# Kernel tuning notes

Hardware: AMD Instinct MI355X
Metric: run time of the kernel (lower is better)

## Reference

```python
import jax, jax.numpy as jnp
import numpy as np

B, N, M = 4, 1024, 4096
DQ, DC = 1024, 1024
H, DH = 16, 64
INNER = H * DH
SCALE = DH ** -0.5


def setup_inputs() -> dict:
    key = jax.random.key(0)
    ks = jax.random.split(key, 6)
    x = jax.random.normal(ks[0], (B, N, DQ), dtype=jnp.float32)
    context = jax.random.normal(ks[1], (B, M, DC), dtype=jnp.float32)
    mask = jax.random.bernoulli(ks[2], 0.9, (B, M))  # bool, True = keep
    # weights, scaled like default torch Linear init (~1/sqrt(fan_in))
    Wq = jax.random.normal(ks[3], (DQ, INNER), dtype=jnp.float32) / np.sqrt(DQ)
    Wkv = jax.random.normal(ks[4], (DC, 2 * INNER), dtype=jnp.float32) / np.sqrt(DC)
    Wo = jax.random.normal(ks[5], (INNER, DQ), dtype=jnp.float32) / np.sqrt(INNER)
    bo = jnp.zeros((DQ,), dtype=jnp.float32)
    return {"x": x, "context": context, "mask": mask,
            "Wq": Wq, "Wkv": Wkv, "Wo": Wo, "bo": bo}


def reference(x, context, mask, Wq, Wkv, Wo, bo):
    # projections
    q = x @ Wq                     # [b, n, h*d]
    kv = context @ Wkv             # [b, m, 2*h*d]
    k, v = jnp.split(kv, 2, axis=-1)
    # split heads: [b, s, h*d] -> [b, h, s, d]
    def heads(t):
        b, s, _ = t.shape
        return t.reshape(b, s, H, DH).transpose(0, 2, 1, 3)
    q, k, v = heads(q), heads(k), heads(v)
    sim = jnp.einsum('bhid,bhjd->bhij', q, k) * SCALE   # [b, h, n, m]
    max_neg = -jnp.finfo(sim.dtype).max
    sim = jnp.where(mask[:, None, None, :], sim, max_neg)
    sim = jnp.clip(sim, -5.0, 5.0)  # masked entries become exactly -5
    attn = jax.nn.softmax(sim, axis=-1)
    out = jnp.einsum('bhij,bhjd->bhid', attn, v)        # [b, h, n, d]
    out = out.transpose(0, 2, 1, 3).reshape(x.shape[0], x.shape[1], INNER)
    return out @ Wo + bo
```

## Files before the change

kernel.cpp:

```cpp
#include <hip/hip_runtime.h>
#include <hip/hip_bf16.h>


typedef __attribute__((ext_vector_type(8))) short short8;
typedef __attribute__((ext_vector_type(8))) unsigned short u16x8;
typedef __attribute__((ext_vector_type(4))) float f32x4;
typedef __attribute__((ext_vector_type(16))) float f32x16;

static __device__ __forceinline__ void gload_lds16(const void* g, void* l) {
  __builtin_amdgcn_global_load_lds((const __attribute__((address_space(1))) void*)g,
                                   (__attribute__((address_space(3))) void*)l, 16, 0, 0);
}

static __device__ __forceinline__ unsigned short f2bf(float f) {
  __hip_bfloat16 h = __float2bfloat16(f);
  unsigned short u;
  __builtin_memcpy(&u, &h, 2);
  return u;
}

static __device__ __forceinline__ float bf2f(unsigned short u) {
  unsigned int x = (unsigned int)u << 16;
  float f;
  __builtin_memcpy(&f, &x, 4);
  return f;
}

static __device__ __forceinline__ unsigned int pack_rnd(float a, float b) {
  unsigned int ua, ub;
  __builtin_memcpy(&ua, &a, 4);
  __builtin_memcpy(&ub, &b, 4);
  return __builtin_amdgcn_perm(ua + 0x8000u, ub + 0x8000u, 0x03020706u);
}

__global__ __launch_bounds__(256) void cast_bf16_kernel(const float* __restrict__ in,
                                                        unsigned short* __restrict__ out,
                                                        int n8) {
  int idx = blockIdx.x * 256 + threadIdx.x;
  int stride = gridDim.x * 256;
  for (int i = idx; i < n8; i += stride) {
    const float4* p = (const float4*)in + (size_t)i * 2;
    float4 a = p[0], b = p[1];
    u16x8 r;
    r[0] = f2bf(a.x); r[1] = f2bf(a.y); r[2] = f2bf(a.z); r[3] = f2bf(a.w);
    r[4] = f2bf(b.x); r[5] = f2bf(b.y); r[6] = f2bf(b.z); r[7] = f2bf(b.w);
    *((u16x8*)out + i) = r;
  }
}

__global__ __launch_bounds__(256) void mask_bias_kernel(const int* __restrict__ mask,
                                                        float* __restrict__ bias, int n) {
  int i = blockIdx.x * 256 + threadIdx.x;
  if (i < n) bias[i] = mask[i] ? 0.0f : -1e30f;
}

__global__ __launch_bounds__(256) void transpose_cast_kernel(const float* __restrict__ W,
                                                             unsigned short* __restrict__ Wt,
                                                             int K, int N) {
  __shared__ float tile[32][33];
  int n0 = blockIdx.x * 32, k0 = blockIdx.y * 32;
  int tx = threadIdx.x & 31, ty = threadIdx.x >> 5;
#pragma unroll
  for (int r = 0; r < 32; r += 8)
    tile[ty + r][tx] = W[(size_t)(k0 + ty + r) * N + n0 + tx];
  __syncthreads();
#pragma unroll
  for (int r = 0; r < 32; r += 8)
    Wt[(size_t)(n0 + ty + r) * K + k0 + tx] = f2bf(tile[tx][ty + r]);
}

template <int EPI>
__global__ __launch_bounds__(256, 2) void gemm_bt_kernel(
    const unsigned short* __restrict__ A, const unsigned short* __restrict__ Bt,
    int M, int N, int K,
    unsigned short* __restrict__ out0, unsigned short* __restrict__ out1,
    float* __restrict__ outF, const float* __restrict__ bias) {
  __shared__ unsigned short As[128 * 64];
  __shared__ unsigned short Bs[128 * 64];
  const int tid = threadIdx.x;
  const int l = tid & 63;
  const int lq = l & 15, g = l >> 4;
  const int w = tid >> 6;
  const int wr = w >> 1, wc = w & 1;
  const int nwg = gridDim.x * gridDim.y;
  const int idl = blockIdx.y * gridDim.x + blockIdx.x;
  const int lin = (idl & 7) * (nwg >> 3) + (idl >> 3);
  const int m0 = (lin / gridDim.x) * 128, n0 = (lin % gridDim.x) * 128;

  f32x4 acc[4][4] = {};

  for (int k0 = 0; k0 < K; k0 += 64) {
    __syncthreads();
#pragma unroll
    for (int t = 0; t < 4; ++t) {
      int c = t * 256 + tid;
      int row = c >> 3, cb = c & 7;
      int srcoff = (cb * 16) ^ ((row & 7) << 4);
      char* la = (char*)As + t * 4096 + (tid & 192) * 16;
      gload_lds16((const char*)(A + (size_t)(m0 + row) * K + k0) + srcoff, la);
      char* lb = (char*)Bs + t * 4096 + (tid & 192) * 16;
      gload_lds16((const char*)(Bt + (size_t)(n0 + row) * K + k0) + srcoff, lb);
    }
    __syncthreads();
#pragma unroll
    for (int ks = 0; ks < 2; ++ks) {
      short8 af[4], bfr[4];
#pragma unroll
      for (int mt = 0; mt < 4; ++mt) {
        int row = wr * 64 + mt * 16 + lq;
        af[mt] = *(const short8*)&As[row * 64 + ((ks * 32 + g * 8) ^ ((row & 7) << 3))];
      }
#pragma unroll
      for (int nt = 0; nt < 4; ++nt) {
        int row = wc * 64 + nt * 16 + lq;
        bfr[nt] = *(const short8*)&Bs[row * 64 + ((ks * 32 + g * 8) ^ ((row & 7) << 3))];
      }
#pragma unroll
      for (int mt = 0; mt < 4; ++mt)
#pragma unroll
        for (int nt = 0; nt < 4; ++nt)
          acc[mt][nt] =
              __builtin_amdgcn_mfma_f32_16x16x32_bf16(af[mt], bfr[nt], acc[mt][nt], 0, 0, 0);
    }
  }

#pragma unroll
  for (int mt = 0; mt < 4; ++mt) {
#pragma unroll
    for (int nt = 0; nt < 4; ++nt) {
      if (EPI == 1 && n0 >= 1024) {
        int colb = n0 - 1024 + wc * 64 + nt * 16 + lq;
        int h = colb >> 6, d = colb & 63;
        int rowb = m0 + wr * 64 + mt * 16 + g * 4;
        int b = rowb >> 12, mm = rowb & 4095;
        ushort4 pk;
        pk.x = f2bf(acc[mt][nt][0]);
        pk.y = f2bf(acc[mt][nt][1]);
        pk.z = f2bf(acc[mt][nt][2]);
        pk.w = f2bf(acc[mt][nt][3]);
        size_t off = (((size_t)(b * 16 + h) * 512 + (mm >> 3)) * 64 + d) * 8 + (mm & 7);
        *(ushort4*)&out1[off] = pk;
      } else {
#pragma unroll
        for (int r = 0; r < 4; ++r) {
          int row = m0 + wr * 64 + mt * 16 + g * 4 + r;
          int col = n0 + wc * 64 + nt * 16 + lq;
          float v = acc[mt][nt][r];
          if (EPI == 0) {
            int b = row >> 10, nq = row & 1023;
            int h = col >> 6, d = col & 63;
            out0[(((size_t)(b * 16 + h)) * 1024 + nq) * 64 + d] =
                f2bf(v * 0.18033688011112042f);
          } else if (EPI == 1) {
            int b = row >> 12, mm = row & 4095;
            int h = col >> 6, d = col & 63;
            size_t off = (((size_t)(b * 16 + h) * 8 + (d >> 3)) * 4096 + mm) * 8 + (d & 7);
            out0[off] = f2bf(v);
          } else {
            outF[(size_t)row * 1024 + col] = v + bias[col];
          }
        }
      }
    }
  }
}

__global__ __launch_bounds__(256, 3) void attn_kernel(
    const unsigned short* __restrict__ K2, const unsigned short* __restrict__ V2,
    const unsigned short* __restrict__ Q, const float* __restrict__ maskb,
    unsigned short* __restrict__ numP, float* __restrict__ denP) {
  __shared__ unsigned short Ks[8 * 128 * 8];
  __shared__ unsigned short Vt[16 * 64 * 8];

  const int tid = threadIdx.x;
  const int l = tid & 63, w = tid >> 6;
  const int lq = l & 31;
  const int hi = l >> 5;

  const int id = blockIdx.x;
  const int xcd = id & 7;
  const int kk = id >> 3;
  const int qi = kk & 7;
  const int pr = xcd * 32 + (kk >> 3);
  const int bh = pr & 63, js = pr >> 6;
  const int b = bh >> 4;
  const int q0 = qi * 128 + w * 32;

  const unsigned short* Qh = Q + (size_t)bh * 1024 * 64;
  const unsigned short* Kh = K2 + (size_t)bh * 8 * 4096 * 8;
  const unsigned short* Vh = V2 + (size_t)bh * 512 * 64 * 8;
  const float* bb = maskb + b * 4096;

  const float CLIP2 = 7.213475204444817f;

  short8 qf[4];
#pragma unroll
  for (int kc = 0; kc < 4; ++kc)
    qf[kc] = *(const short8*)&Qh[(size_t)(q0 + lq) * 64 + kc * 16 + hi * 8];

  f32x16 oacc[2] = {};
  float den = 0.f;

  for (int jt = js * 8; jt < js * 8 + 8; ++jt) {
    const int j0 = jt * 128;
    __syncthreads();
#pragma unroll
    for (int t = 0; t < 4; ++t) {
      int c = t * 256 + tid;
      int db = c >> 7, jj = c & 127;
      int sig = (jj & ~12) | ((jj & 4) << 1) | ((jj & 8) >> 1);
      char* lk = (char*)Ks + t * 4096 + (tid & 192) * 16;
      gload_lds16((const char*)(Kh + ((size_t)db * 4096 + j0 + sig) * 8), lk);
    }
#pragma unroll
    for (int t = 0; t < 4; ++t) {
      int c = t * 256 + tid;
      int jb = c >> 6, d = c & 63;
      char* lv = (char*)Vt + t * 4096 + (tid & 192) * 16;
      gload_lds16((const char*)(Vh + ((size_t)((j0 >> 3) + jb) * 64 + d) * 8), lv);
    }
    __syncthreads();

#pragma unroll
    for (int half = 0; half < 4; ++half) {
      f32x16 sacc;
#pragma unroll
      for (int bq = 0; bq < 4; ++bq) {
        f32x4 m4 = *(const f32x4*)&bb[j0 + half * 32 + ((bq & 1) << 2) + (hi << 3) +
                                      ((bq >> 1) << 4)];
        sacc[bq * 4 + 0] = m4[0];
        sacc[bq * 4 + 1] = m4[1];
        sacc[bq * 4 + 2] = m4[2];
        sacc[bq * 4 + 3] = m4[3];
      }
      __builtin_amdgcn_s_setprio(1);
#pragma unroll
      for (int kc = 0; kc < 4; ++kc) {
        short8 kf = *(const short8*)((const char*)Ks + (2 * kc + hi) * 2048 +
                                     (half * 32 + lq) * 16);
        sacc = __builtin_amdgcn_mfma_f32_32x32x16_bf16(kf, qf[kc], sacc, 0, 0, 0);
      }
      __builtin_amdgcn_s_setprio(0);
#pragma unroll
      for (int r = 0; r < 16; ++r) {
        float v = __builtin_amdgcn_fmed3f(sacc[r], -CLIP2, CLIP2);
        float p = exp2f(v);
        sacc[r] = p;
        den += p;
      }
      unsigned int wds[8];
#pragma unroll
      for (int i = 0; i < 8; ++i) wds[i] = pack_rnd(sacc[i * 2], sacc[i * 2 + 1]);
      __builtin_amdgcn_s_setprio(1);
#pragma unroll
      for (int kt = 0; kt < 2; ++kt) {
        union { unsigned int u[4]; short8 s; } pa;
        pa.u[0] = wds[kt * 4 + 0];
        pa.u[1] = wds[kt * 4 + 1];
        pa.u[2] = wds[kt * 4 + 2];
        pa.u[3] = wds[kt * 4 + 3];
#pragma unroll
        for (int dt = 0; dt < 2; ++dt) {
          short8 vf = *(const short8*)((const char*)Vt +
              (4 * half + 2 * kt + hi) * 1024 + (dt * 32 + lq) * 16);
          oacc[dt] = __builtin_amdgcn_mfma_f32_32x32x16_bf16(pa.s, vf, oacc[dt], 0, 0, 0);
        }
      }
      __builtin_amdgcn_s_setprio(0);
    }
  }

  den += __shfl_xor(den, 32);
  if (l < 32) denP[(((size_t)js * 64 + bh) * 1024) + q0 + l] = den;

#pragma unroll
  for (int dt = 0; dt < 2; ++dt)
#pragma unroll
    for (int r = 0; r < 16; ++r) {
      int q = q0 + (r & 3) + 8 * (r >> 2) + 4 * hi;
      int d = dt * 32 + lq;
      numP[((((size_t)js * 64 + bh) * 1024 + q) * 64) + d] = f2bf(oacc[dt][r]);
    }
}

__global__ __launch_bounds__(256) void attn_reduce_kernel(
    const unsigned short* __restrict__ numP, const float* __restrict__ denP,
    unsigned short* __restrict__ Ob) {
  int id = blockIdx.x * 256 + threadIdx.x;
  int d8 = id & 7;
  int q = (id >> 3) & 1023;
  int bh = id >> 13;
  int b = bh >> 4, h = bh & 15;
  float den = 0.f;
  float o[8] = {0.f, 0.f, 0.f, 0.f, 0.f, 0.f, 0.f, 0.f};
#pragma unroll
  for (int s = 0; s < 4; ++s) {
    const unsigned short* np =
        numP + ((((size_t)s * 64 + bh) * 1024 + q) * 64 + d8 * 8);
    u16x8 v = *(const u16x8*)np;
    den += denP[((size_t)s * 64 + bh) * 1024 + q];
#pragma unroll
    for (int e = 0; e < 8; ++e) o[e] += bf2f(v[e]);
  }
  float r = 1.0f / den;
  u16x8 outv;
#pragma unroll
  for (int e = 0; e < 8; ++e) outv[e] = f2bf(o[e] * r);
  *(u16x8*)&Ob[(((size_t)b * 1024 + q) * 1024) + h * 64 + d8 * 8] = outv;
}

extern "C" void kernel_launch(void* const* d_in, const int* in_sizes, int n_in,
                              void* d_out, int out_size, void* d_ws, size_t ws_size,
                              hipStream_t stream) {
  (void)in_sizes; (void)n_in; (void)out_size; (void)ws_size;
  const float* x    = (const float*)d_in[0];
  const float* ctx  = (const float*)d_in[1];
  const int*   mask = (const int*)d_in[2];
  const float* Wq   = (const float*)d_in[3];
  const float* Wkv  = (const float*)d_in[4];
  const float* Wo   = (const float*)d_in[5];
  const float* bo   = (const float*)d_in[6];
  float* out = (float*)d_out;

  char* ws = (char*)d_ws;
  const size_t MB = 1 << 20;
  unsigned short* numP = (unsigned short*)(ws + 0);
  float*          denP = (float*)(ws + 32 * MB);
  float*          mbias= (float*)(ws + 33 * MB);
  unsigned short* xb   = (unsigned short*)(ws + 0);
  unsigned short* cb   = (unsigned short*)(ws + 8 * MB);
  unsigned short* WqT  = (unsigned short*)(ws + 40 * MB);
  unsigned short* WkvT = (unsigned short*)(ws + 42 * MB);
  unsigned short* WoT  = (unsigned short*)(ws + 46 * MB);
  unsigned short* Qb   = (unsigned short*)(ws + 48 * MB);
  unsigned short* K2   = (unsigned short*)(ws + 56 * MB);
  unsigned short* V2   = (unsigned short*)(ws + 88 * MB);
  unsigned short* Ob   = (unsigned short*)(ws + 120 * MB);

  cast_bf16_kernel<<<2048, 256, 0, stream>>>(x, xb, (4 * 1024 * 1024) / 8);
  cast_bf16_kernel<<<2048, 256, 0, stream>>>(ctx, cb, (16 * 1024 * 1024) / 8);
  transpose_cast_kernel<<<dim3(32, 32), 256, 0, stream>>>(Wq, WqT, 1024, 1024);
  transpose_cast_kernel<<<dim3(64, 32), 256, 0, stream>>>(Wkv, WkvT, 1024, 2048);
  transpose_cast_kernel<<<dim3(32, 32), 256, 0, stream>>>(Wo, WoT, 1024, 1024);

  gemm_bt_kernel<0><<<dim3(8, 32), 256, 0, stream>>>(xb, WqT, 4096, 1024, 1024,
                                                     Qb, (unsigned short*)nullptr,
                                                     (float*)nullptr, (const float*)nullptr);
  gemm_bt_kernel<1><<<dim3(16, 128), 256, 0, stream>>>(cb, WkvT, 16384, 2048, 1024,
                                                       K2, V2,
                                                       (float*)nullptr, (const float*)nullptr);
  mask_bias_kernel<<<64, 256, 0, stream>>>(mask, mbias, 4 * 4096);
  attn_kernel<<<2048, 256, 0, stream>>>(K2, V2, Qb, mbias, numP, denP);
  attn_reduce_kernel<<<2048, 256, 0, stream>>>(numP, denP, Ob);
  gemm_bt_kernel<2><<<dim3(8, 32), 256, 0, stream>>>(Ob, WoT, 4096, 1024, 1024,
                                                     (unsigned short*)nullptr, (unsigned short*)nullptr,
                                                     out, bo);
}
```

Measured before the change: 259.8 us.

## Double-buffer K/V tiles in LDS with 64-key stages and use native exp2

Splits the attention key loop into 64-key tiles held in two LDS buffers, so the next tile is fetched asynchronously while the current one is computed. Each iteration now needs one barrier instead of two, and the same total LDS is kept. It also swaps exp2f for the hardware exp2 builtin to drop the range-handling code. Smaller tiles mean more loop iterations and barriers, and the native exp2 may lose a little accuracy on denormals.

```diff
diff --git a/kernel.cpp b/kernel.cpp
--- a/kernel.cpp
+++ b/kernel.cpp
@@ -169,8 +169,8 @@
     const unsigned short* __restrict__ K2, const unsigned short* __restrict__ V2,
     const unsigned short* __restrict__ Q, const float* __restrict__ maskb,
     unsigned short* __restrict__ numP, float* __restrict__ denP) {
-  __shared__ unsigned short Ks[8 * 128 * 8];
-  __shared__ unsigned short Vt[16 * 64 * 8];
+  __shared__ unsigned short Ks[2][8 * 64 * 8];
+  __shared__ unsigned short Vt[2][8 * 64 * 8];
 
   const int tid = threadIdx.x;
   const int l = tid & 63, w = tid >> 6;
@@ -201,28 +201,34 @@
   f32x16 oacc[2] = {};
   float den = 0.f;
 
-  for (int jt = js * 8; jt < js * 8 + 8; ++jt) {
-    const int j0 = jt * 128;
-    __syncthreads();
-#pragma unroll
-    for (int t = 0; t < 4; ++t) {
-      int c = t * 256 + tid;
-      int db = c >> 7, jj = c & 127;
-      int sig = (jj & ~12) | ((jj & 4) << 1) | ((jj & 8) >> 1);
-      char* lk = (char*)Ks + t * 4096 + (tid & 192) * 16;
-      gload_lds16((const char*)(Kh + ((size_t)db * 4096 + j0 + sig) * 8), lk);
-    }
-#pragma unroll
-    for (int t = 0; t < 4; ++t) {
-      int c = t * 256 + tid;
-      int jb = c >> 6, d = c & 63;
-      char* lv = (char*)Vt + t * 4096 + (tid & 192) * 16;
-      gload_lds16((const char*)(Vh + ((size_t)((j0 >> 3) + jb) * 64 + d) * 8), lv);
-    }
-    __syncthreads();
-
-#pragma unroll
-    for (int half = 0; half < 4; ++half) {
+  const int jbeg = js * 16, jend = jbeg + 16;
+
+#define STAGE_KV(bi_, j0_)                                                       \
+  do {                                                                           \
+    _Pragma("unroll") for (int t = 0; t < 2; ++t) {                              \
+      int c = t * 256 + tid;                                                     \
+      int db = c >> 6, jj = c & 63;                                              \
+      int sig = (jj & 0x33) | ((jj & 4) << 1) | ((jj & 8) >> 1);                 \
+      char* lk = (char*)(&Ks[bi_][0]) + t * 4096 + (tid & 192) * 16;             \
+      gload_lds16((const char*)(Kh + ((size_t)db * 4096 + (j0_) + sig) * 8), lk);\
+      char* lv = (char*)(&Vt[bi_][0]) + t * 4096 + (tid & 192) * 16;             \
+      gload_lds16((const char*)(Vh + ((size_t)(((j0_) >> 3) + db) * 64 + jj) * 8), lv); \
+    }                                                                            \
+  } while (0)
+
+  STAGE_KV(0, jbeg * 64);
+  __syncthreads();
+
+  for (int jt = jbeg; jt < jend; ++jt) {
+    const int j0 = jt * 64;
+    const int cur = jt & 1;
+    if (jt + 1 < jend) STAGE_KV(cur ^ 1, j0 + 64);
+
+    const unsigned short* Kc = &Ks[cur][0];
+    const unsigned short* Vc = &Vt[cur][0];
+
+#pragma unroll
+    for (int half = 0; half < 2; ++half) {
       f32x16 sacc;
 #pragma unroll
       for (int bq = 0; bq < 4; ++bq) {
@@ -236,7 +242,7 @@
       __builtin_amdgcn_s_setprio(1);
 #pragma unroll
       for (int kc = 0; kc < 4; ++kc) {
-        short8 kf = *(const short8*)((const char*)Ks + (2 * kc + hi) * 2048 +
+        short8 kf = *(const short8*)((const char*)Kc + (2 * kc + hi) * 1024 +
                                      (half * 32 + lq) * 16);
         sacc = __builtin_amdgcn_mfma_f32_32x32x16_bf16(kf, qf[kc], sacc, 0, 0, 0);
       }
@@ -244,7 +250,7 @@
 #pragma unroll
       for (int r = 0; r < 16; ++r) {
         float v = __builtin_amdgcn_fmed3f(sacc[r], -CLIP2, CLIP2);
-        float p = exp2f(v);
+        float p = __builtin_amdgcn_exp2f(v);
         sacc[r] = p;
         den += p;
       }
@@ -261,14 +267,16 @@
         pa.u[3] = wds[kt * 4 + 3];
 #pragma unroll
         for (int dt = 0; dt < 2; ++dt) {
-          short8 vf = *(const short8*)((const char*)Vt +
+          short8 vf = *(const short8*)((const char*)Vc +
               (4 * half + 2 * kt + hi) * 1024 + (dt * 32 + lq) * 16);
           oacc[dt] = __builtin_amdgcn_mfma_f32_32x32x16_bf16(pa.s, vf, oacc[dt], 0, 0, 0);
         }
       }
       __builtin_amdgcn_s_setprio(0);
     }
-  }
+    __syncthreads();
+  }
+#undef STAGE_KV
 
   den += __shfl_xor(den, 32);
   if (l < 32) denP[(((size_t)js * 64 + bh) * 1024) + q0 + l] = den;
```

Result: faster. 243.2 us (-6.4%).
